# Kernel tuning notes

Measured on AMD Instinct MI355X. Metric: run time of the kernel, lower is better.

The kernel has to match this reference:

```python
import jax, jax.numpy as jnp
import numpy as np

B, S, D, H = 2, 2048, 1024, 16
DK = D // H


def setup_inputs() -> dict:
    key = jax.random.key(0)
    ks = jax.random.split(key, 8)
    scale = 1.0 / np.sqrt(D)
    return {
        "Q": jax.random.normal(ks[0], (B, S, D), jnp.float32),
        "K": jax.random.normal(ks[1], (B, S, D), jnp.float32),
        "V": jax.random.normal(ks[2], (B, S, D), jnp.float32),
        "Wq": jax.random.normal(ks[3], (D, D), jnp.float32) * scale,
        "Wk": jax.random.normal(ks[4], (D, D), jnp.float32) * scale,
        "Wv": jax.random.normal(ks[5], (D, D), jnp.float32) * scale,
        "Wo": jax.random.normal(ks[6], (D, D), jnp.float32) * scale,
        "bo": jax.random.normal(ks[7], (D,), jnp.float32) * 0.01,
    }


def reference(Q, K, V, Wq, Wk, Wv, Wo, bo):
    # Projections: [B,S,D] @ [D,D]
    q = (Q @ Wq).reshape(B, S, H, DK).transpose(0, 2, 1, 3)  # [B,H,S,dk]
    k = (K @ Wk).reshape(B, S, H, DK).transpose(0, 2, 1, 3)
    v = (V @ Wv).reshape(B, S, H, DK).transpose(0, 2, 1, 3)
    scores = jnp.einsum("bhsd,bhtd->bhst", q, k) / jnp.sqrt(jnp.float32(DK))
    # causal mask (masked=True): disallow t > s
    causal = jnp.tril(jnp.ones((S, S), dtype=bool))  # True = keep
    scores = jnp.where(causal[None, None], scores, -jnp.inf)
    attn = jax.nn.softmax(scores, axis=-1)
    out = jnp.einsum("bhst,bhtd->bhsd", attn, v)  # [B,H,S,dk]
    out = out.transpose(0, 2, 1, 3).reshape(B, S, D)
    return out @ Wo + bo
```

## Files before the change

### kernel.cpp

```cpp
#include <hip/hip_runtime.h>
#include <hip/hip_bf16.h>

typedef unsigned short ushort_t;
typedef __attribute__((ext_vector_type(8))) short short8;
typedef __attribute__((ext_vector_type(4))) float f32x4;
typedef __attribute__((ext_vector_type(2))) unsigned int uint2v;

#define B_  2
#define S_  2048
#define D_  1024
#define H_  16
#define DK_ 64

#define NEG_BIG (-1e30f)
#define SCALE2 0.18033688011112042f

__device__ __forceinline__ void async16(const void* g, void* l) {
  __builtin_amdgcn_global_load_lds((const __attribute__((address_space(1))) void*)g,
                                   (__attribute__((address_space(3))) void*)l, 16, 0, 0);
}
__device__ __forceinline__ ushort_t f2bf(float x) {
  __hip_bfloat16 h = __float2bfloat16(x);
  ushort_t u; __builtin_memcpy(&u, &h, 2); return u;
}
__device__ __forceinline__ unsigned int pack_bf2(float lo, float hi) {
  __hip_bfloat162 h2 = __float22bfloat162_rn(make_float2(lo, hi));
  unsigned int u; __builtin_memcpy(&u, &h2, 4); return u;
}

__global__ __launch_bounds__(256) void prep(const float* Q, const float* K, const float* V,
                                            const float* W0, const float* W1,
                                            const float* W2, const float* W3,
                                            ushort_t* qb, ushort_t* kb, ushort_t* vb,
                                            ushort_t* Wt) {
  __shared__ float tile[64][65];
  int z = blockIdx.z;
  if (z < 3) {
    const float* src = (z == 0) ? Q : (z == 1) ? K : V;
    ushort_t* dst = (z == 0) ? qb : (z == 1) ? kb : vb;
    size_t i = ((size_t)blockIdx.x * 256 + threadIdx.x) * 8;
    f32x4 a = *(const f32x4*)(src + i);
    f32x4 b = *(const f32x4*)(src + i + 4);
    short8 p;
    p[0] = (short)f2bf(a[0]); p[1] = (short)f2bf(a[1]);
    p[2] = (short)f2bf(a[2]); p[3] = (short)f2bf(a[3]);
    p[4] = (short)f2bf(b[0]); p[5] = (short)f2bf(b[1]);
    p[6] = (short)f2bf(b[2]); p[7] = (short)f2bf(b[3]);
    *(short8*)(dst + i) = p;
  } else {
    if (blockIdx.x >= 256) return;
    int zz = z - 3;
    const float* W = (zz == 0) ? W0 : (zz == 1) ? W1 : (zz == 2) ? W2 : W3;
    ushort_t* O = Wt + (size_t)zz * D_ * D_;
    int bx = blockIdx.x & 15, by = blockIdx.x >> 4;
    int tx = threadIdx.x & 63, ty = threadIdx.x >> 6;
    int r0 = by * 64, c0 = bx * 64;
    for (int i = 0; i < 16; i++) {
      int r = ty + i * 4;
      tile[r][tx] = W[(size_t)(r0 + r) * D_ + c0 + tx];
    }
    __syncthreads();
    for (int i = 0; i < 16; i++) {
      int r = ty + i * 4;
      O[(size_t)(c0 + r) * D_ + r0 + tx] = f2bf(tile[tx][r]);
    }
  }
}

template <int NT>
__device__ __forceinline__ void gemm_core_t(const ushort_t* A, const ushort_t* Bt,
                                            int bm, int bn, f32x4 acc[4][NT],
                                            ushort_t* As, ushort_t* Bs,
                                            int lane, int w, int wm, int wn) {
  int l16 = lane & 15, quad = lane >> 4;
  for (int mi = 0; mi < 4; mi++)
    for (int ni = 0; ni < NT; ni++) acc[mi][ni] = (f32x4){0.f, 0.f, 0.f, 0.f};
  int arow = lane >> 2, aseg = (lane & 3) * 8;
  for (int k0 = 0; k0 < D_; k0 += 32) {
    __syncthreads();
    for (int j = 0; j < 2; j++) {
      int rb = w * 32 + j * 16;
      async16(A + (size_t)(bm + rb + arow) * D_ + k0 + aseg, As + rb * 32);
    }
    for (int j = 0; j < NT / 2; j++) {
      int rb = w * 16 * (NT / 2) + j * 16;
      async16(Bt + (size_t)(bn + rb + arow) * D_ + k0 + aseg, Bs + rb * 32);
    }
    __syncthreads();
    short8 af[4], bfv[NT];
    for (int mi = 0; mi < 4; mi++)
      af[mi] = *(const short8*)(As + (wm + mi * 16 + l16) * 32 + quad * 8);
    for (int ni = 0; ni < NT; ni++)
      bfv[ni] = *(const short8*)(Bs + (wn + ni * 16 + l16) * 32 + quad * 8);
    for (int mi = 0; mi < 4; mi++)
      for (int ni = 0; ni < NT; ni++)
        acc[mi][ni] = __builtin_amdgcn_mfma_f32_16x16x32_bf16(af[mi], bfv[ni], acc[mi][ni], 0, 0, 0);
  }
}

__global__ __launch_bounds__(256) void qkv_proj(const ushort_t* qb, const ushort_t* kb,
                                                const ushort_t* vb, const ushort_t* Wt,
                                                ushort_t* qh, ushort_t* kh, ushort_t* vT) {
  __shared__ alignas(16) ushort_t As[128 * 32];
  __shared__ alignas(16) ushort_t Bs[128 * 32];
  int tid = threadIdx.x, lane = tid & 63, w = tid >> 6;
  int wm = (w & 1) * 64, wn = (w >> 1) * 64;
  int bm = blockIdx.y * 128, bn = blockIdx.x * 128;
  int z = blockIdx.z;
  const ushort_t* A = (z == 0) ? qb : (z == 1) ? kb : vb;
  const ushort_t* Bt = Wt + (size_t)z * D_ * D_;
  f32x4 acc[4][4];
  gemm_core_t<4>(A, Bt, bm, bn, acc, As, Bs, lane, w, wm, wn);
  int l16 = lane & 15, quad = lane >> 4;
  float qscale = (z == 0) ? SCALE2 : 1.0f;
  for (int mi = 0; mi < 4; mi++)
    for (int ni = 0; ni < 4; ni++)
      for (int r = 0; r < 4; r++) {
        int row = bm + wm + mi * 16 + quad * 4 + r;
        int col = bn + wn + ni * 16 + l16;
        int b = row >> 11, s = row & (S_ - 1);
        int h = col >> 6, dk = col & 63;
        float v = acc[mi][ni][r] * qscale;
        if (z == 2)
          vT[((size_t)(b * H_ + h) * DK_ + dk) * S_ + s] = f2bf(v);
        else {
          ushort_t* dst = (z == 0) ? qh : kh;
          dst[((size_t)(b * H_ + h) * S_ + s) * DK_ + dk] = f2bf(v);
        }
      }
}

__global__ __launch_bounds__(256) void out_proj(const ushort_t* A, const ushort_t* Wt,
                                                const float* bias, float* C) {
  __shared__ alignas(16) ushort_t As[128 * 32];
  __shared__ alignas(16) ushort_t Bs[64 * 32];
  int tid = threadIdx.x, lane = tid & 63, w = tid >> 6;
  int wm = (w & 1) * 64, wn = (w >> 1) * 32;
  int bm = blockIdx.y * 128, bn = blockIdx.x * 64;
  f32x4 acc[4][2];
  gemm_core_t<2>(A, Wt, bm, bn, acc, As, Bs, lane, w, wm, wn);
  int l16 = lane & 15, quad = lane >> 4;
  for (int ni = 0; ni < 2; ni++) {
    int col = bn + wn + ni * 16 + l16;
    float bv = bias[col];
    for (int mi = 0; mi < 4; mi++)
      for (int r = 0; r < 4; r++) {
        int row = bm + wm + mi * 16 + quad * 4 + r;
        C[(size_t)row * D_ + col] = acc[mi][ni][r] + bv;
      }
  }
}

__global__ __launch_bounds__(256) void flash_attn(const ushort_t* qh, const ushort_t* kh,
                                                  const ushort_t* vT, ushort_t* outO) {
  __shared__ alignas(16) ushort_t Ks[2][64 * 64];
  __shared__ alignas(16) ushort_t Vs[2][64 * 64];
  __shared__ alignas(16) ushort_t Ps[4][16 * 72];
  int tid = threadIdx.x, lane = tid & 63, w = tid >> 6;
  int l16 = lane & 15, quad = lane >> 4;
  int p = blockIdx.x >> 5;
  int bh = blockIdx.x & 31;
  int b = bh >> 4, h = bh & 15;
  const ushort_t* qb = qh + (size_t)bh * S_ * DK_;
  const ushort_t* kb = kh + (size_t)bh * S_ * DK_;
  const ushort_t* vb = vT + (size_t)bh * DK_ * S_;
  ushort_t* ps = Ps[w];
  int srow = lane >> 3;
  int lseg8 = ((lane & 7) ^ srow) * 8;
  int swz = l16 & 7;
  int wrow = w * 16;

  int buf = 0;
  for (int half = 0; half < 2; half++) {
    int j = half ? p : (31 - p);
    int qs = j * 64;
    int nt = j + 1;
    short8 qf[2];
    {
      const ushort_t* qp = qb + (size_t)(qs + wrow + l16) * DK_;
      qf[0] = *(const short8*)(qp + quad * 8);
      qf[1] = *(const short8*)(qp + 32 + quad * 8);
    }
    float l_part = 0.f;
    f32x4 o[4];
    for (int f = 0; f < 4; f++) o[f] = (f32x4){0.f, 0.f, 0.f, 0.f};
    for (int jj = 0; jj < 2; jj++) {
      int rb = w * 16 + jj * 8;
      async16(kb + (size_t)(rb + srow) * DK_ + lseg8, Ks[buf] + rb * 64);
      async16(vb + (size_t)(rb + srow) * S_ + lseg8, Vs[buf] + rb * 64);
    }
    for (int it = 0; it < nt; it++) {
      int t0 = it << 6;
      __syncthreads();
      if (it + 1 < nt) {
        int t1 = t0 + 64, nb = buf ^ 1;
        for (int jj = 0; jj < 2; jj++) {
          int rb = w * 16 + jj * 8;
          async16(kb + (size_t)(t1 + rb + srow) * DK_ + lseg8, Ks[nb] + rb * 64);
          async16(vb + (size_t)(rb + srow) * S_ + t1 + lseg8, Vs[nb] + rb * 64);
        }
      }
      const ushort_t* Kb = Ks[buf];
      const ushort_t* Vb = Vs[buf];
      f32x4 sf[4];
      for (int f = 0; f < 4; f++) sf[f] = (f32x4){0.f, 0.f, 0.f, 0.f};
      for (int st = 0; st < 2; st++) {
        short8 kfr[4];
        for (int f = 0; f < 4; f++)
          kfr[f] = *(const short8*)(Kb + (f * 16 + l16) * 64 + (((st * 4 + quad) ^ swz) * 8));
        for (int f = 0; f < 4; f++)
          sf[f] = __builtin_amdgcn_mfma_f32_16x16x32_bf16(kfr[f], qf[st], sf[f], 0, 0, 0);
      }
      if (it == nt - 1) {
        int s = qs + wrow + l16;
        for (int f = 0; f < 4; f++) {
          int tb = t0 + f * 16 + quad * 4;
          for (int r = 0; r < 4; r++)
            if (tb + r > s) sf[f][r] = NEG_BIG;
        }
      }
      for (int f = 0; f < 4; f++)
        for (int r = 0; r < 4; r++) {
          float pv = exp2f(sf[f][r]);
          sf[f][r] = pv;
          l_part += pv;
        }
      for (int f = 0; f < 4; f++) {
        uint2v pk;
        pk.x = pack_bf2(sf[f][0], sf[f][1]);
        pk.y = pack_bf2(sf[f][2], sf[f][3]);
        *(uint2v*)(ps + l16 * 72 + f * 16 + quad * 4) = pk;
      }
      asm volatile("s_waitcnt lgkmcnt(0)" ::: "memory");
      for (int st = 0; st < 2; st++) {
        short8 vfr[4];
        for (int f = 0; f < 4; f++)
          vfr[f] = *(const short8*)(Vb + (f * 16 + l16) * 64 + (((st * 4 + quad) ^ swz) * 8));
        short8 pf = *(const short8*)(ps + l16 * 72 + st * 32 + quad * 8);
        for (int f = 0; f < 4; f++)
          o[f] = __builtin_amdgcn_mfma_f32_16x16x32_bf16(vfr[f], pf, o[f], 0, 0, 0);
      }
      buf ^= 1;
    }
    float l_r = l_part;
    l_r += __shfl_xor(l_r, 16, 64);
    l_r += __shfl_xor(l_r, 32, 64);
    float inv = 1.0f / l_r;
    int s = qs + wrow + l16;
    ushort_t* op = outO + (size_t)(b * S_ + s) * D_ + h * DK_;
    for (int f = 0; f < 4; f++) {
      uint2v pk;
      pk.x = pack_bf2(o[f][0] * inv, o[f][1] * inv);
      pk.y = pack_bf2(o[f][2] * inv, o[f][3] * inv);
      *(uint2v*)(op + f * 16 + quad * 4) = pk;
    }
  }
}

extern "C" void kernel_launch(void* const* d_in, const int* in_sizes, int n_in,
                              void* d_out, int out_size, void* d_ws, size_t ws_size,
                              hipStream_t stream) {
  const float* Q  = (const float*)d_in[0];
  const float* K  = (const float*)d_in[1];
  const float* V  = (const float*)d_in[2];
  const float* Wq = (const float*)d_in[3];
  const float* Wk = (const float*)d_in[4];
  const float* Wv = (const float*)d_in[5];
  const float* Wo = (const float*)d_in[6];
  const float* bo = (const float*)d_in[7];
  ushort_t* ws = (ushort_t*)d_ws;
  ushort_t* Wt = ws;
  ushort_t* qb = ws + ((size_t)4 << 20);
  ushort_t* kb = ws + ((size_t)8 << 20);
  ushort_t* vb = ws + ((size_t)12 << 20);
  ushort_t* qh = ws + ((size_t)16 << 20);
  ushort_t* kh = ws + ((size_t)20 << 20);
  ushort_t* vT = ws + ((size_t)24 << 20);
  ushort_t* aO = qb;

  prep<<<dim3(2048, 1, 7), 256, 0, stream>>>(Q, K, V, Wq, Wk, Wv, Wo, qb, kb, vb, Wt);
  qkv_proj<<<dim3(8, 32, 3), 256, 0, stream>>>(qb, kb, vb, Wt, qh, kh, vT);
  flash_attn<<<512, 256, 0, stream>>>(qh, kh, vT, aO);
  out_proj<<<dim3(16, 32, 1), 256, 0, stream>>>(aO, Wt + ((size_t)3 << 20), bo, (float*)d_out);
}
```

Measured before the change: 220.3 us.

## Stage V-transpose stores through LDS and split flash attention into one tile per block

In the QKV projection, the V output is first transposed in shared memory and then written to vT as coalesced 16-byte rows, replacing scattered 2-byte strided stores. The flash-attention kernel no longer pairs a long and a short query tile per block. It launches 1024 blocks, each handling one 64-row query tile, with heavy tiles scheduled first. This gives more parallelism, at the cost of losing the built-in load balancing from pairing and adding an extra round of Q loads and epilogues.

After: 207.9 us. -5.6%, faster.

```diff
diff --git a/kernel.cpp b/kernel.cpp
--- a/kernel.cpp
+++ b/kernel.cpp
@@ -101,8 +101,9 @@
 __global__ __launch_bounds__(256) void qkv_proj(const ushort_t* qb, const ushort_t* kb,
                                                 const ushort_t* vb, const ushort_t* Wt,
                                                 ushort_t* qh, ushort_t* kh, ushort_t* vT) {
-  __shared__ alignas(16) ushort_t As[128 * 32];
-  __shared__ alignas(16) ushort_t Bs[128 * 32];
+  __shared__ alignas(16) ushort_t Sh[8704];
+  ushort_t* As = Sh;
+  ushort_t* Bs = Sh + 4096;
   int tid = threadIdx.x, lane = tid & 63, w = tid >> 6;
   int wm = (w & 1) * 64, wn = (w >> 1) * 64;
   int bm = blockIdx.y * 128, bn = blockIdx.x * 128;
@@ -112,22 +113,38 @@
   f32x4 acc[4][4];
   gemm_core_t<4>(A, Bt, bm, bn, acc, As, Bs, lane, w, wm, wn);
   int l16 = lane & 15, quad = lane >> 4;
-  float qscale = (z == 0) ? SCALE2 : 1.0f;
-  for (int mi = 0; mi < 4; mi++)
-    for (int ni = 0; ni < 4; ni++)
-      for (int r = 0; r < 4; r++) {
-        int row = bm + wm + mi * 16 + quad * 4 + r;
-        int col = bn + wn + ni * 16 + l16;
-        int b = row >> 11, s = row & (S_ - 1);
-        int h = col >> 6, dk = col & 63;
-        float v = acc[mi][ni][r] * qscale;
-        if (z == 2)
-          vT[((size_t)(b * H_ + h) * DK_ + dk) * S_ + s] = f2bf(v);
-        else {
-          ushort_t* dst = (z == 0) ? qh : kh;
-          dst[((size_t)(b * H_ + h) * S_ + s) * DK_ + dk] = f2bf(v);
+  if (z == 2) {
+    int b = bm >> 11, s0 = bm & (S_ - 1);
+    for (int p = 0; p < 2; p++) {
+      __syncthreads();
+      if ((w >> 1) == p) {
+        for (int mi = 0; mi < 4; mi++)
+          for (int ni = 0; ni < 4; ni++)
+            for (int r = 0; r < 4; r++)
+              Sh[(ni * 16 + l16) * 136 + wm + mi * 16 + quad * 4 + r] = f2bf(acc[mi][ni][r]);
+      }
+      __syncthreads();
+      for (int c = tid; c < 1024; c += 256) {
+        int row = c >> 4, seg = c & 15;
+        int colg = bn + p * 64 + row;
+        int h = colg >> 6, dk = colg & 63;
+        short8 t = *(const short8*)(Sh + row * 136 + seg * 8);
+        *(short8*)(vT + ((size_t)(b * H_ + h) * DK_ + dk) * S_ + s0 + seg * 8) = t;
+      }
+    }
+  } else {
+    float qscale = (z == 0) ? SCALE2 : 1.0f;
+    ushort_t* dst = (z == 0) ? qh : kh;
+    for (int mi = 0; mi < 4; mi++)
+      for (int ni = 0; ni < 4; ni++)
+        for (int r = 0; r < 4; r++) {
+          int row = bm + wm + mi * 16 + quad * 4 + r;
+          int col = bn + wn + ni * 16 + l16;
+          int b = row >> 11, s = row & (S_ - 1);
+          int h = col >> 6, dk = col & 63;
+          dst[((size_t)(b * H_ + h) * S_ + s) * DK_ + dk] = f2bf(acc[mi][ni][r] * qscale);
         }
-      }
+  }
 }
 
 __global__ __launch_bounds__(256) void out_proj(const ushort_t* A, const ushort_t* Wt,
@@ -158,9 +175,11 @@
   __shared__ alignas(16) ushort_t Ps[4][16 * 72];
   int tid = threadIdx.x, lane = tid & 63, w = tid >> 6;
   int l16 = lane & 15, quad = lane >> 4;
-  int p = blockIdx.x >> 5;
+  int j = 31 - (int)(blockIdx.x >> 5);
   int bh = blockIdx.x & 31;
   int b = bh >> 4, h = bh & 15;
+  int qs = j * 64;
+  int nt = j + 1;
   const ushort_t* qb = qh + (size_t)bh * S_ * DK_;
   const ushort_t* kb = kh + (size_t)bh * S_ * DK_;
   const ushort_t* vb = vT + (size_t)bh * DK_ * S_;
@@ -170,90 +189,86 @@
   int swz = l16 & 7;
   int wrow = w * 16;
 
+  short8 qf[2];
+  {
+    const ushort_t* qp = qb + (size_t)(qs + wrow + l16) * DK_;
+    qf[0] = *(const short8*)(qp + quad * 8);
+    qf[1] = *(const short8*)(qp + 32 + quad * 8);
+  }
+  float l_part = 0.f;
+  f32x4 o[4];
+  for (int f = 0; f < 4; f++) o[f] = (f32x4){0.f, 0.f, 0.f, 0.f};
+
   int buf = 0;
-  for (int half = 0; half < 2; half++) {
-    int j = half ? p : (31 - p);
-    int qs = j * 64;
-    int nt = j + 1;
-    short8 qf[2];
-    {
-      const ushort_t* qp = qb + (size_t)(qs + wrow + l16) * DK_;
-      qf[0] = *(const short8*)(qp + quad * 8);
-      qf[1] = *(const short8*)(qp + 32 + quad * 8);
-    }
-    float l_part = 0.f;
-    f32x4 o[4];
-    for (int f = 0; f < 4; f++) o[f] = (f32x4){0.f, 0.f, 0.f, 0.f};
-    for (int jj = 0; jj < 2; jj++) {
-      int rb = w * 16 + jj * 8;
-      async16(kb + (size_t)(rb + srow) * DK_ + lseg8, Ks[buf] + rb * 64);
-      async16(vb + (size_t)(rb + srow) * S_ + lseg8, Vs[buf] + rb * 64);
-    }
-    for (int it = 0; it < nt; it++) {
-      int t0 = it << 6;
-      __syncthreads();
-      if (it + 1 < nt) {
-        int t1 = t0 + 64, nb = buf ^ 1;
-        for (int jj = 0; jj < 2; jj++) {
-          int rb = w * 16 + jj * 8;
-          async16(kb + (size_t)(t1 + rb + srow) * DK_ + lseg8, Ks[nb] + rb * 64);
-          async16(vb + (size_t)(rb + srow) * S_ + t1 + lseg8, Vs[nb] + rb * 64);
-        }
-      }
-      const ushort_t* Kb = Ks[buf];
-      const ushort_t* Vb = Vs[buf];
-      f32x4 sf[4];
-      for (int f = 0; f < 4; f++) sf[f] = (f32x4){0.f, 0.f, 0.f, 0.f};
-      for (int st = 0; st < 2; st++) {
-        short8 kfr[4];
-        for (int f = 0; f < 4; f++)
-          kfr[f] = *(const short8*)(Kb + (f * 16 + l16) * 64 + (((st * 4 + quad) ^ swz) * 8));
-        for (int f = 0; f < 4; f++)
-          sf[f] = __builtin_amdgcn_mfma_f32_16x16x32_bf16(kfr[f], qf[st], sf[f], 0, 0, 0);
-      }
-      if (it == nt - 1) {
-        int s = qs + wrow + l16;
-        for (int f = 0; f < 4; f++) {
-          int tb = t0 + f * 16 + quad * 4;
-          for (int r = 0; r < 4; r++)
-            if (tb + r > s) sf[f][r] = NEG_BIG;
-        }
-      }
+  for (int jj = 0; jj < 2; jj++) {
+    int rb = w * 16 + jj * 8;
+    async16(kb + (size_t)(rb + srow) * DK_ + lseg8, Ks[0] + rb * 64);
+    async16(vb + (size_t)(rb + srow) * S_ + lseg8, Vs[0] + rb * 64);
+  }
+  for (int it = 0; it < nt; it++) {
+    int t0 = it << 6;
+    __syncthreads();
+    if (it + 1 < nt) {
+      int t1 = t0 + 64, nb = buf ^ 1;
+      for (int jj = 0; jj < 2; jj++) {
+        int rb = w * 16 + jj * 8;
+        async16(kb + (size_t)(t1 + rb + srow) * DK_ + lseg8, Ks[nb] + rb * 64);
+        async16(vb + (size_t)(rb + srow) * S_ + t1 + lseg8, Vs[nb] + rb * 64);
+      }
+    }
+    const ushort_t* Kb = Ks[buf];
+    const ushort_t* Vb = Vs[buf];
+    f32x4 sf[4];
+    for (int f = 0; f < 4; f++) sf[f] = (f32x4){0.f, 0.f, 0.f, 0.f};
+    for (int st = 0; st < 2; st++) {
+      short8 kfr[4];
       for (int f = 0; f < 4; f++)
-        for (int r = 0; r < 4; r++) {
-          float pv = exp2f(sf[f][r]);
-          sf[f][r] = pv;
-          l_part += pv;
-        }
+        kfr[f] = *(const short8*)(Kb + (f * 16 + l16) * 64 + (((st * 4 + quad) ^ swz) * 8));
+      for (int f = 0; f < 4; f++)
+        sf[f] = __builtin_amdgcn_mfma_f32_16x16x32_bf16(kfr[f], qf[st], sf[f], 0, 0, 0);
+    }
+    if (it == nt - 1) {
+      int s = qs + wrow + l16;
       for (int f = 0; f < 4; f++) {
-        uint2v pk;
-        pk.x = pack_bf2(sf[f][0], sf[f][1]);
-        pk.y = pack_bf2(sf[f][2], sf[f][3]);
-        *(uint2v*)(ps + l16 * 72 + f * 16 + quad * 4) = pk;
-      }
-      asm volatile("s_waitcnt lgkmcnt(0)" ::: "memory");
-      for (int st = 0; st < 2; st++) {
-        short8 vfr[4];
-        for (int f = 0; f < 4; f++)
-          vfr[f] = *(const short8*)(Vb + (f * 16 + l16) * 64 + (((st * 4 + quad) ^ swz) * 8));
-        short8 pf = *(const short8*)(ps + l16 * 72 + st * 32 + quad * 8);
-        for (int f = 0; f < 4; f++)
-          o[f] = __builtin_amdgcn_mfma_f32_16x16x32_bf16(vfr[f], pf, o[f], 0, 0, 0);
-      }
-      buf ^= 1;
-    }
-    float l_r = l_part;
-    l_r += __shfl_xor(l_r, 16, 64);
-    l_r += __shfl_xor(l_r, 32, 64);
-    float inv = 1.0f / l_r;
-    int s = qs + wrow + l16;
-    ushort_t* op = outO + (size_t)(b * S_ + s) * D_ + h * DK_;
+        int tb = t0 + f * 16 + quad * 4;
+        for (int r = 0; r < 4; r++)
+          if (tb + r > s) sf[f][r] = NEG_BIG;
+      }
+    }
+    for (int f = 0; f < 4; f++)
+      for (int r = 0; r < 4; r++) {
+        float pv = exp2f(sf[f][r]);
+        sf[f][r] = pv;
+        l_part += pv;
+      }
     for (int f = 0; f < 4; f++) {
       uint2v pk;
-      pk.x = pack_bf2(o[f][0] * inv, o[f][1] * inv);
-      pk.y = pack_bf2(o[f][2] * inv, o[f][3] * inv);
-      *(uint2v*)(op + f * 16 + quad * 4) = pk;
-    }
+      pk.x = pack_bf2(sf[f][0], sf[f][1]);
+      pk.y = pack_bf2(sf[f][2], sf[f][3]);
+      *(uint2v*)(ps + l16 * 72 + f * 16 + quad * 4) = pk;
+    }
+    asm volatile("s_waitcnt lgkmcnt(0)" ::: "memory");
+    for (int st = 0; st < 2; st++) {
+      short8 vfr[4];
+      for (int f = 0; f < 4; f++)
+        vfr[f] = *(const short8*)(Vb + (f * 16 + l16) * 64 + (((st * 4 + quad) ^ swz) * 8));
+      short8 pf = *(const short8*)(ps + l16 * 72 + st * 32 + quad * 8);
+      for (int f = 0; f < 4; f++)
+        o[f] = __builtin_amdgcn_mfma_f32_16x16x32_bf16(vfr[f], pf, o[f], 0, 0, 0);
+    }
+    buf ^= 1;
+  }
+  float l_r = l_part;
+  l_r += __shfl_xor(l_r, 16, 64);
+  l_r += __shfl_xor(l_r, 32, 64);
+  float inv = 1.0f / l_r;
+  int s = qs + wrow + l16;
+  ushort_t* op = outO + (size_t)(b * S_ + s) * D_ + h * DK_;
+  for (int f = 0; f < 4; f++) {
+    uint2v pk;
+    pk.x = pack_bf2(o[f][0] * inv, o[f][1] * inv);
+    pk.y = pack_bf2(o[f][2] * inv, o[f][3] * inv);
+    *(uint2v*)(op + f * 16 + quad * 4) = pk;
   }
 }
 
@@ -280,6 +295,6 @@
 
   prep<<<dim3(2048, 1, 7), 256, 0, stream>>>(Q, K, V, Wq, Wk, Wv, Wo, qb, kb, vb, Wt);
   qkv_proj<<<dim3(8, 32, 3), 256, 0, stream>>>(qb, kb, vb, Wt, qh, kh, vT);
-  flash_attn<<<512, 256, 0, stream>>>(qh, kh, vT, aO);
+  flash_attn<<<1024, 256, 0, stream>>>(qh, kh, vT, aO);
   out_proj<<<dim3(16, 32, 1), 256, 0, stream>>>(aO, Wt + ((size_t)3 << 20), bo, (float*)d_out);
 }
```
